# Performance work log

Measured on AMD Instinct MI355X. Metric: run time of the kernel, lower is better.

Reference implementation:

```python
import jax, jax.numpy as jnp
import numpy as np

N, E, D_IN, D, L = 50000, 800000, 128, 256, 3
BN_EPS = 1e-5


def _bn(x, gamma, beta):
    # torch BatchNorm1d training-mode forward: biased batch statistics over node dim
    m = x.mean(axis=0)
    v = x.var(axis=0)  # ddof=0, matches torch normalization
    return gamma * (x - m) * jax.lax.rsqrt(v + BN_EPS) + beta


def setup_inputs() -> dict:
    key = jax.random.key(0)
    ks = jax.random.split(key, 12)
    s_in = 1.0 / np.sqrt(D_IN)
    s_d = 1.0 / np.sqrt(D)
    s_2d = 1.0 / np.sqrt(2 * D)
    return {
        "pre_node_emb": jax.random.normal(ks[0], (1, N, D_IN), jnp.float32),
        "edge_index": jax.random.randint(ks[1], (1, E, 2), 0, N, jnp.int64),
        "W0": jax.random.uniform(ks[2], (D_IN, D), jnp.float32, -s_in, s_in),
        "b0": jax.random.uniform(ks[3], (D,), jnp.float32, -s_in, s_in),
        "W1": jax.random.uniform(ks[4], (L, D, 2 * D), jnp.float32, -s_d, s_d),
        "b1": jax.random.uniform(ks[5], (L, 2 * D), jnp.float32, -s_d, s_d),
        "g1": jnp.ones((L, 2 * D), jnp.float32),
        "beta1": jnp.zeros((L, 2 * D), jnp.float32),
        "W2": jax.random.uniform(ks[6], (L, 2 * D, D), jnp.float32, -s_2d, s_2d),
        "b2": jax.random.uniform(ks[7], (L, D), jnp.float32, -s_2d, s_2d),
        "gf": jnp.ones((L, D), jnp.float32),
        "betaf": jnp.zeros((L, D), jnp.float32),
    }


def reference(pre_node_emb, edge_index, W0, b0, W1, b1, g1, beta1, W2, b2, gf, betaf):
    x = pre_node_emb[0]            # [N, D_IN]
    ei = edge_index[0]             # [E, 2] -> transposed in torch; rows are (src, dst)
    src, dst = ei[:, 0], ei[:, 1]
    x = x @ W0 + b0                # node embedder -> [N, D]
    for l in range(L):
        # GINConv (eps=0): sum-aggregate neighbor messages, then MLP
        agg = jax.ops.segment_sum(x[src], dst, num_segments=N)   # scatter-add
        h = x + agg
        h = h @ W1[l] + b1[l]
        h = _bn(h, g1[l], beta1[l])
        h = jax.nn.relu(h)
        h = h @ W2[l] + b2[l]
        x = _bn(h + x, gf[l], betaf[l])  # residual + outer BatchNorm
    return x
```

## Files before the change

### kernel.cpp

```cpp
#include <hip/hip_runtime.h>

#define MNODES 50000
#define M_PAD  50048
#define NEDGES 800000
#define DIN    128
#define DD     256
#define D2     512
#define NLAYERS 3
#define BN_EPS 1e-5f
#define NREP   16

typedef unsigned short ushort_t;
typedef __bf16 v8bf __attribute__((ext_vector_type(8)));
typedef unsigned short v8us __attribute__((ext_vector_type(8)));
typedef float  v4f  __attribute__((ext_vector_type(4)));

#define GLOBAL_AS __attribute__((address_space(1)))
#define LDS_AS    __attribute__((address_space(3)))

__device__ __forceinline__ float bf2f(ushort_t u) {
    unsigned x = ((unsigned)u) << 16;
    return __uint_as_float(x);
}
__device__ __forceinline__ ushort_t f2bf(float f) {
    unsigned u = __float_as_uint(f);
    u += 0x7FFF + ((u >> 16) & 1);
    return (ushort_t)(u >> 16);
}
__device__ __forceinline__ void async16(const ushort_t* g, ushort_t* l) {
    __builtin_amdgcn_global_load_lds((const GLOBAL_AS unsigned int*)g,
                                     (LDS_AS unsigned int*)l, 16, 0, 0);
}
#define BARRIER() asm volatile("s_barrier" ::: "memory")
#define VMWAIT4() asm volatile("s_waitcnt vmcnt(4)" ::: "memory")
#define VMWAIT0() asm volatile("s_waitcnt vmcnt(0)" ::: "memory")
#define LGKM0()   asm volatile("s_waitcnt lgkmcnt(0)" ::: "memory")

#define R0 (M_PAD * DIN)
#define RW (DIN * DD + 2 * NLAYERS * DD * D2)
#define NSTATZ (NREP * D2 * 2 + NREP * DD * 2)
__global__ void k_prep_all(const float* __restrict__ pre, ushort_t* __restrict__ preb,
                           const float* __restrict__ W0, const float* __restrict__ W1,
                           const float* __restrict__ W2,
                           ushort_t* __restrict__ W0T, ushort_t* __restrict__ W1T,
                           ushort_t* __restrict__ W2T,
                           float* __restrict__ caf, float* __restrict__ ccf,
                           float* __restrict__ statz, int* __restrict__ deg) {
    int i = blockIdx.x * blockDim.x + threadIdx.x;
    if (i < R0) {
        int row = i >> 7;
        preb[i] = f2bf(row < MNODES ? pre[i] : 0.f);
        return;
    }
    int j = i - R0;
    if (j < RW) {
        if (j < DIN * DD) {
            int n = j >> 7, k = j & 127;
            W0T[j] = f2bf(W0[k * DD + n]);
        } else if (j < DIN * DD + NLAYERS * DD * D2) {
            int j2 = j - DIN * DD;
            int l = j2 >> 17, off = j2 & 131071;
            int n = off >> 8, k = off & 255;
            W1T[(size_t)l * 131072 + off] = f2bf(W1[(size_t)l * 131072 + k * D2 + n]);
        } else {
            int j2 = j - DIN * DD - NLAYERS * DD * D2;
            int l = j2 >> 17, off = j2 & 131071;
            int n = off >> 9, k = off & 511;
            W2T[(size_t)l * 131072 + off] = f2bf(W2[(size_t)l * 131072 + k * DD + n]);
        }
        return;
    }
    j -= RW;
    if (j < 256) { caf[j] = 1.f; ccf[j] = 0.f; return; }
    j -= 256;
    if (j < NSTATZ) { statz[j] = 0.f; return; }
    j -= NSTATZ;
    if (j < MNODES) deg[j] = 0;
}

__global__ void k_hist(const int* __restrict__ ei, int* __restrict__ deg) {
    int e = blockIdx.x * blockDim.x + threadIdx.x;
    if (e < NEDGES) atomicAdd(&deg[ei[e * 2 + 1]], 1);
}
__global__ void k_scan1(const int* __restrict__ deg, int* __restrict__ rowptr,
                        int* __restrict__ bsum, int n) {
    __shared__ int tmp[256];
    int tid = threadIdx.x;
    int i = blockIdx.x * 256 + tid;
    int v = (i < n) ? deg[i] : 0;
    tmp[tid] = v;
    __syncthreads();
    #pragma unroll
    for (int off = 1; off < 256; off <<= 1) {
        int t = (tid >= off) ? tmp[tid - off] : 0;
        __syncthreads();
        tmp[tid] += t;
        __syncthreads();
    }
    if (i < n) rowptr[i + 1] = tmp[tid];
    if (tid == 255) bsum[blockIdx.x] = tmp[255];
}
__global__ __launch_bounds__(256)
void k_scan2(int* __restrict__ bsum, int nb) {
    __shared__ int tmp[256];
    int tid = threadIdx.x;
    int v = (tid < nb) ? bsum[tid] : 0;
    tmp[tid] = v;
    __syncthreads();
    #pragma unroll
    for (int off = 1; off < 256; off <<= 1) {
        int t = (tid >= off) ? tmp[tid - off] : 0;
        __syncthreads();
        tmp[tid] += t;
        __syncthreads();
    }
    if (tid < nb) bsum[tid] = tmp[tid] - v;
}
__global__ void k_scan3(const int* __restrict__ deg, const int* __restrict__ bsum,
                        int* __restrict__ rowptr, int* __restrict__ cursor, int n) {
    int i = blockIdx.x * 256 + threadIdx.x;
    if (i == 0) rowptr[0] = 0;
    if (i < n) {
        int incl = rowptr[i + 1] + bsum[i >> 8];
        rowptr[i + 1] = incl;
        cursor[i] = incl - deg[i];
    }
}
__global__ void k_fill(const int* __restrict__ ei, int* __restrict__ cursor,
                       int* __restrict__ col) {
    int e = blockIdx.x * blockDim.x + threadIdx.x;
    if (e < NEDGES) {
        int pos = atomicAdd(&cursor[ei[e * 2 + 1]], 1);
        col[pos] = ei[e * 2];
    }
}

__global__ void k_gather(const int* __restrict__ rowptr, const int* __restrict__ col,
                         const ushort_t* __restrict__ x, const float* __restrict__ ca,
                         const float* __restrict__ cc, ushort_t* __restrict__ out) {
    int node = blockIdx.x * 4 + (threadIdx.x >> 6);
    int lane = threadIdx.x & 63;
    if (node >= MNODES) return;
    const ushort4* xp = (const ushort4*)x;
    ushort4 v = xp[(size_t)node * 64 + lane];
    float a0 = bf2f(v.x), a1 = bf2f(v.y), a2 = bf2f(v.z), a3 = bf2f(v.w);
    int s = rowptr[node], e = rowptr[node + 1];
    int i = s;
    for (; i + 7 < e; i += 8) {
        ushort4 u[8];
        #pragma unroll
        for (int j = 0; j < 8; j++) u[j] = xp[(size_t)col[i + j] * 64 + lane];
        #pragma unroll
        for (int j = 0; j < 8; j++) {
            a0 += bf2f(u[j].x); a1 += bf2f(u[j].y);
            a2 += bf2f(u[j].z); a3 += bf2f(u[j].w);
        }
    }
    for (; i < e; i++) {
        ushort4 u = xp[(size_t)col[i] * 64 + lane];
        a0 += bf2f(u.x); a1 += bf2f(u.y); a2 += bf2f(u.z); a3 += bf2f(u.w);
    }
    int c = lane * 4;
    float dn = (float)(e - s) + 1.0f;
    ushort4 o;
    o.x = f2bf(ca[c + 0] * a0 + dn * cc[c + 0]);
    o.y = f2bf(ca[c + 1] * a1 + dn * cc[c + 1]);
    o.z = f2bf(ca[c + 2] * a2 + dn * cc[c + 2]);
    o.w = f2bf(ca[c + 3] * a3 + dn * cc[c + 3]);
    ((ushort4*)out)[(size_t)node * 64 + lane] = o;
}

__global__ void k_coeffs(float* __restrict__ sums, float* __restrict__ sumsq,
                         const float* __restrict__ g, const float* __restrict__ beta,
                         float* __restrict__ ca, float* __restrict__ cc,
                         float2* __restrict__ cacc, int n) {
    int c = blockIdx.x * blockDim.x + threadIdx.x;
    if (c >= n) return;
    float s = 0.f, q = 0.f;
    #pragma unroll
    for (int r = 0; r < NREP; r++) {
        s += sums[r * n + c];  sums[r * n + c]  = 0.f;
        q += sumsq[r * n + c]; sumsq[r * n + c] = 0.f;
    }
    float mean = s * (1.0f / MNODES);
    float var  = q * (1.0f / MNODES) - mean * mean;
    float a    = g[c] * rsqrtf(var + BN_EPS);
    float b    = beta[c] - a * mean;
    ca[c] = a;
    cc[c] = b;
    if (cacc) cacc[c] = make_float2(a, b);
}

__global__ void k_apply_out(const ushort_t* __restrict__ h, const float* __restrict__ ca,
                            const float* __restrict__ cc, float* __restrict__ out) {
    int i = blockIdx.x * blockDim.x + threadIdx.x;
    if (i >= MNODES * 64) return;
    int c = (i & 63) * 4;
    ushort4 v = ((const ushort4*)h)[i];
    float4 o;
    o.x = ca[c + 0] * bf2f(v.x) + cc[c + 0];
    o.y = ca[c + 1] * bf2f(v.y) + cc[c + 1];
    o.z = ca[c + 2] * bf2f(v.z) + cc[c + 2];
    o.w = ca[c + 3] * bf2f(v.w) + cc[c + 3];
    ((float4*)out)[i] = o;
}

template<int DO_STATS, int RES, int FUSE_BN>
__global__ __launch_bounds__(256, 4)
void k_gemm_bf(const ushort_t* __restrict__ A, const ushort_t* __restrict__ WT,
               const float* __restrict__ bias,
               const ushort_t* resid, const float* __restrict__ r_ca,
               const float* __restrict__ r_cc, const float2* __restrict__ cacc,
               ushort_t* out, float* __restrict__ sums, float* __restrict__ sumsq,
               int M, int K, int N) {
    __shared__ __align__(16) ushort_t As[2][128 * 32];
    __shared__ __align__(16) ushort_t Bs[2][128 * 32];
    const int tid = threadIdx.x;
    const int w = tid >> 6, lane = tid & 63;
    const int wm = w >> 1, wn = w & 1;
    const int quad = lane >> 4, l15 = lane & 15;

    const int nxb = N >> 7;
    const int nwg = nxb * (int)gridDim.y;
    const int orig = (int)blockIdx.y * nxb + (int)blockIdx.x;
    const int qq = nwg >> 3, rr = nwg & 7, xc = orig & 7, oi = orig >> 3;
    const int swz = (xc < rr ? xc * (qq + 1) : rr * (qq + 1) + (xc - rr) * qq) + oi;
    const int bx = swz & (nxb - 1);
    const int by = (nxb == 4) ? (swz >> 2) : (swz >> 1);
    const int m0 = by * 128, n0 = bx * 128;

    float2* cacc_lds = nullptr;
    if constexpr (FUSE_BN != 0) {
        __shared__ __align__(16) float2 cacc_s[512];
        cacc_lds = cacc_s;
        for (int k2 = tid; k2 < K; k2 += 256) cacc_lds[k2] = cacc[k2];
        LGKM0();
    }

    const ushort_t* aA[2];
    const ushort_t* aB[2];
    int aoff[2];
    #pragma unroll
    for (int j = 0; j < 2; j++) {
        int ii = j * 4 + w;
        int r = ii * 16 + (lane >> 2);
        int cg = (lane & 3) ^ ((r >> 2) & 3);
        aA[j] = A  + (size_t)(m0 + r) * K + cg * 8;
        aB[j] = WT + (size_t)(n0 + r) * K + cg * 8;
        aoff[j] = ii * 512;
    }

    v4f acc[4][4];
    #pragma unroll
    for (int i = 0; i < 4; i++)
        #pragma unroll
        for (int j = 0; j < 4; j++)
            acc[i][j] = (v4f){0.f, 0.f, 0.f, 0.f};

    const int nk = K >> 5;

    #pragma unroll
    for (int j = 0; j < 2; j++) {
        async16(aA[j], &As[0][aoff[j]]);
        async16(aB[j], &Bs[0][aoff[j]]);
    }
    #pragma unroll
    for (int j = 0; j < 2; j++) {
        async16(aA[j] + 32, &As[1][aoff[j]]);
        async16(aB[j] + 32, &Bs[1][aoff[j]]);
    }
    VMWAIT4();
    BARRIER();

    const int sl = quad ^ ((l15 >> 2) & 3);
    for (int t = 0; t < nk; t++) {
        const ushort_t* Ab = As[t & 1];
        const ushort_t* Bb = Bs[t & 1];
        v8bf af[4], bfr[4];
        #pragma unroll
        for (int tt = 0; tt < 4; tt++) {
            int m_l = wm * 64 + tt * 16 + l15;
            af[tt]  = *(const v8bf*)&Ab[m_l * 32 + sl * 8];
            int n_l = wn * 64 + tt * 16 + l15;
            bfr[tt] = *(const v8bf*)&Bb[n_l * 32 + sl * 8];
        }
        if constexpr (FUSE_BN != 0) {
            const float* cb = (const float*)&cacc_lds[(t << 5) + (quad << 3)];
            float cav[8], ccv[8];
            #pragma unroll
            for (int j = 0; j < 8; j++) { cav[j] = cb[2 * j]; ccv[j] = cb[2 * j + 1]; }
            #pragma unroll
            for (int tt = 0; tt < 4; tt++) {
                v8us au = *(v8us*)&af[tt];
                v8us ou;
                #pragma unroll
                for (int j = 0; j < 8; j++) {
                    float h = bf2f(au[j]);
                    ou[j] = f2bf(fmaxf(fmaf(cav[j], h, ccv[j]), 0.f));
                }
                af[tt] = *(v8bf*)&ou;
            }
        }
        #pragma unroll
        for (int mt = 0; mt < 4; mt++)
            #pragma unroll
            for (int nt = 0; nt < 4; nt++)
                acc[mt][nt] = __builtin_amdgcn_mfma_f32_16x16x32_bf16(
                    af[mt], bfr[nt], acc[mt][nt], 0, 0, 0);
        if (t == nk - 1) break;
        BARRIER();
        if (t + 2 < nk) {
            int kl = (t + 2) * 32;
            #pragma unroll
            for (int j = 0; j < 2; j++) {
                async16(aA[j] + kl, &As[t & 1][aoff[j]]);
                async16(aB[j] + kl, &Bs[t & 1][aoff[j]]);
            }
            VMWAIT4();
        } else {
            VMWAIT0();
        }
        BARRIER();
    }

    const int mlim = M - m0;
    float s_sum[4] = {0.f, 0.f, 0.f, 0.f}, s_sq[4] = {0.f, 0.f, 0.f, 0.f};
    #pragma unroll
    for (int nt = 0; nt < 4; nt++) {
        int colg = n0 + wn * 64 + nt * 16 + l15;
        float bia = bias[colg];
        float rca = 0.f, rcc = 0.f;
        if (RES) { rca = r_ca[colg]; rcc = r_cc[colg]; }
        #pragma unroll
        for (int mt = 0; mt < 4; mt++) {
            int rbase = wm * 64 + mt * 16 + quad * 4;
            #pragma unroll
            for (int r = 0; r < 4; r++) {
                int rl = rbase + r;
                if (rl < mlim) {
                    size_t idx = (size_t)(m0 + rl) * N + colg;
                    float v = acc[mt][nt][r] + bia;
                    if (RES) v += rca * bf2f(resid[idx]) + rcc;
                    out[idx] = f2bf(v);
                    if (DO_STATS) { s_sum[nt] += v; s_sq[nt] += v * v; }
                }
            }
        }
    }
    if (DO_STATS) {
        const int rep = by & (NREP - 1);
        #pragma unroll
        for (int nt = 0; nt < 4; nt++) {
            float s = s_sum[nt], q = s_sq[nt];
            s += __shfl_xor(s, 16); q += __shfl_xor(q, 16);
            s += __shfl_xor(s, 32); q += __shfl_xor(q, 32);
            if (quad == 0) {
                int colg = n0 + wn * 64 + nt * 16 + l15;
                atomicAdd(&sums[rep * N + colg], s);
                atomicAdd(&sumsq[rep * N + colg], q);
            }
        }
    }
}

extern "C" void kernel_launch(void* const* d_in, const int* in_sizes, int n_in,
                              void* d_out, int out_size, void* d_ws, size_t ws_size,
                              hipStream_t stream) {
    const float* pre   = (const float*)d_in[0];
    const int*   ei    = (const int*)d_in[1];
    const float* W0    = (const float*)d_in[2];
    const float* b0    = (const float*)d_in[3];
    const float* W1    = (const float*)d_in[4];
    const float* b1    = (const float*)d_in[5];
    const float* g1    = (const float*)d_in[6];
    const float* beta1 = (const float*)d_in[7];
    const float* W2    = (const float*)d_in[8];
    const float* b2    = (const float*)d_in[9];
    const float* gf    = (const float*)d_in[10];
    const float* betaf = (const float*)d_in[11];

    char* p = (char*)d_ws;
    ushort_t* preb = (ushort_t*)p; p += (size_t)M_PAD * DIN * 2;
    ushort_t* ACT1 = (ushort_t*)p; p += (size_t)M_PAD * DD * 2;
    ushort_t* ACT2 = (ushort_t*)p; p += (size_t)M_PAD * DD * 2;
    ushort_t* H1   = (ushort_t*)p; p += (size_t)M_PAD * D2 * 2;
    ushort_t* W0T  = (ushort_t*)p; p += (size_t)DIN * DD * 2;
    ushort_t* W1T  = (ushort_t*)p; p += (size_t)NLAYERS * DD * D2 * 2;
    ushort_t* W2T  = (ushort_t*)p; p += (size_t)NLAYERS * D2 * DD * 2;
    float* sums1  = (float*)p; p += (size_t)NREP * D2 * 4;
    float* sumsq1 = (float*)p; p += (size_t)NREP * D2 * 4;
    float* sumsF  = (float*)p; p += (size_t)NREP * DD * 4;
    float* sumsqF = (float*)p; p += (size_t)NREP * DD * 4;
    float* ca1    = (float*)p; p += D2 * 4;
    float* cc1    = (float*)p; p += D2 * 4;
    float* caf    = (float*)p; p += DD * 4;
    float* ccf    = (float*)p; p += DD * 4;
    float2* cacc1 = (float2*)p; p += D2 * 8;
    int* deg    = (int*)p; p += (size_t)MNODES * 4;
    int* rowptr = (int*)p; p += (size_t)(MNODES + 1) * 4;
    int* cursor = (int*)p; p += (size_t)MNODES * 4;
    int* colx   = (int*)p; p += (size_t)NEDGES * 4;
    int* bsum   = (int*)p; p += 256 * 4;

    dim3 blk(256);
    const int mb = (MNODES + 127) / 128;
    const int nsb = (MNODES + 255) / 256;

    const int prep_total = R0 + RW + 256 + NSTATZ + MNODES;
    k_prep_all<<<(prep_total + 255) / 256, blk, 0, stream>>>(
        pre, preb, W0, W1, W2, W0T, W1T, W2T, caf, ccf, sums1, deg);

    k_hist<<<(NEDGES + 255) / 256, blk, 0, stream>>>(ei, deg);
    k_scan1<<<nsb, blk, 0, stream>>>(deg, rowptr, bsum, MNODES);
    k_scan2<<<1, blk, 0, stream>>>(bsum, nsb);
    k_scan3<<<nsb, blk, 0, stream>>>(deg, bsum, rowptr, cursor, MNODES);
    k_fill<<<(NEDGES + 255) / 256, blk, 0, stream>>>(ei, cursor, colx);

    k_gemm_bf<0, 0, 0><<<dim3(DD / 128, mb), blk, 0, stream>>>(
        preb, W0T, b0, nullptr, nullptr, nullptr, nullptr,
        ACT2, nullptr, nullptr, MNODES, DIN, DD);

    for (int l = 0; l < NLAYERS; l++) {
        k_gather<<<(MNODES + 3) / 4, blk, 0, stream>>>(rowptr, colx, ACT2, caf, ccf, ACT1);

        k_gemm_bf<1, 0, 0><<<dim3(D2 / 128, mb), blk, 0, stream>>>(
            ACT1, W1T + (size_t)l * DD * D2, b1 + (size_t)l * D2,
            nullptr, nullptr, nullptr, nullptr,
            H1, sums1, sumsq1, MNODES, DD, D2);
        k_coeffs<<<2, blk, 0, stream>>>(sums1, sumsq1, g1 + (size_t)l * D2,
                                        beta1 + (size_t)l * D2, ca1, cc1, cacc1, D2);

        k_gemm_bf<1, 1, 1><<<dim3(DD / 128, mb), blk, 0, stream>>>(
            H1, W2T + (size_t)l * D2 * DD, b2 + (size_t)l * DD,
            ACT2, caf, ccf, cacc1,
            ACT2, sumsF, sumsqF, MNODES, D2, DD);
        k_coeffs<<<1, blk, 0, stream>>>(sumsF, sumsqF, gf + (size_t)l * DD,
                                        betaf + (size_t)l * DD, caf, ccf, nullptr, DD);
    }

    k_apply_out<<<(MNODES * 64 + 255) / 256, blk, 0, stream>>>(ACT2, caf, ccf, (float*)d_out);
}
```

Before: 749.4 us.

## Load GEMM fragments directly from global memory into registers, bypassing LDS

The bf16 MFMA GEMM no longer stages A and B tiles in double-buffered LDS with async global-to-LDS copies and barriers. Each wave now loads its own A and B fragments straight from global memory into registers, with a two-stage register ping-pong for A. K becomes a template parameter so loop bounds and strides are compile-time constants. This removes LDS traffic and barrier synchronisation, but rows shared between waves are loaded redundantly through the caches, B fragments are fetched just before use with little latency hiding, and accesses are less coalesced.

Measured after the change: 1.264 ms. 68.7% more time.

```diff
diff --git a/kernel.cpp b/kernel.cpp
--- a/kernel.cpp
+++ b/kernel.cpp
@@ -15,9 +15,6 @@
 typedef unsigned short v8us __attribute__((ext_vector_type(8)));
 typedef float  v4f  __attribute__((ext_vector_type(4)));
 
-#define GLOBAL_AS __attribute__((address_space(1)))
-#define LDS_AS    __attribute__((address_space(3)))
-
 __device__ __forceinline__ float bf2f(ushort_t u) {
     unsigned x = ((unsigned)u) << 16;
     return __uint_as_float(x);
@@ -27,13 +24,6 @@
     u += 0x7FFF + ((u >> 16) & 1);
     return (ushort_t)(u >> 16);
 }
-__device__ __forceinline__ void async16(const ushort_t* g, ushort_t* l) {
-    __builtin_amdgcn_global_load_lds((const GLOBAL_AS unsigned int*)g,
-                                     (LDS_AS unsigned int*)l, 16, 0, 0);
-}
-#define BARRIER() asm volatile("s_barrier" ::: "memory")
-#define VMWAIT4() asm volatile("s_waitcnt vmcnt(4)" ::: "memory")
-#define VMWAIT0() asm volatile("s_waitcnt vmcnt(0)" ::: "memory")
 #define LGKM0()   asm volatile("s_waitcnt lgkmcnt(0)" ::: "memory")
 
 #define R0 (M_PAD * DIN)
@@ -205,16 +195,14 @@
     ((float4*)out)[i] = o;
 }
 
-template<int DO_STATS, int RES, int FUSE_BN>
+template<int DO_STATS, int RES, int FUSE_BN, int KT>
 __global__ __launch_bounds__(256, 4)
 void k_gemm_bf(const ushort_t* __restrict__ A, const ushort_t* __restrict__ WT,
                const float* __restrict__ bias,
                const ushort_t* resid, const float* __restrict__ r_ca,
                const float* __restrict__ r_cc, const float2* __restrict__ cacc,
                ushort_t* out, float* __restrict__ sums, float* __restrict__ sumsq,
-               int M, int K, int N) {
-    __shared__ __align__(16) ushort_t As[2][128 * 32];
-    __shared__ __align__(16) ushort_t Bs[2][128 * 32];
+               int M, int N) {
     const int tid = threadIdx.x;
     const int w = tid >> 6, lane = tid & 63;
     const int wm = w >> 1, wn = w & 1;
@@ -231,24 +219,15 @@
 
     float2* cacc_lds = nullptr;
     if constexpr (FUSE_BN != 0) {
-        __shared__ __align__(16) float2 cacc_s[512];
+        __shared__ __align__(16) float2 cacc_s[KT];
         cacc_lds = cacc_s;
-        for (int k2 = tid; k2 < K; k2 += 256) cacc_lds[k2] = cacc[k2];
-        LGKM0();
-    }
-
-    const ushort_t* aA[2];
-    const ushort_t* aB[2];
-    int aoff[2];
-    #pragma unroll
-    for (int j = 0; j < 2; j++) {
-        int ii = j * 4 + w;
-        int r = ii * 16 + (lane >> 2);
-        int cg = (lane & 3) ^ ((r >> 2) & 3);
-        aA[j] = A  + (size_t)(m0 + r) * K + cg * 8;
-        aB[j] = WT + (size_t)(n0 + r) * K + cg * 8;
-        aoff[j] = ii * 512;
-    }
+        #pragma unroll
+        for (int k2 = tid; k2 < KT; k2 += 256) cacc_lds[k2] = cacc[k2];
+        __syncthreads();
+    }
+
+    const ushort_t* Ap = A  + (size_t)(m0 + wm * 64 + l15) * KT + quad * 8;
+    const ushort_t* Bp = WT + (size_t)(n0 + wn * 64 + l15) * KT + quad * 8;
 
     v4f acc[4][4];
     #pragma unroll
@@ -257,48 +236,31 @@
         for (int j = 0; j < 4; j++)
             acc[i][j] = (v4f){0.f, 0.f, 0.f, 0.f};
 
-    const int nk = K >> 5;
-
-    #pragma unroll
-    for (int j = 0; j < 2; j++) {
-        async16(aA[j], &As[0][aoff[j]]);
-        async16(aB[j], &Bs[0][aoff[j]]);
-    }
-    #pragma unroll
-    for (int j = 0; j < 2; j++) {
-        async16(aA[j] + 32, &As[1][aoff[j]]);
-        async16(aB[j] + 32, &Bs[1][aoff[j]]);
-    }
-    VMWAIT4();
-    BARRIER();
-
-    const int sl = quad ^ ((l15 >> 2) & 3);
-    for (int t = 0; t < nk; t++) {
-        const ushort_t* Ab = As[t & 1];
-        const ushort_t* Bb = Bs[t & 1];
-        v8bf af[4], bfr[4];
-        #pragma unroll
-        for (int tt = 0; tt < 4; tt++) {
-            int m_l = wm * 64 + tt * 16 + l15;
-            af[tt]  = *(const v8bf*)&Ab[m_l * 32 + sl * 8];
-            int n_l = wn * 64 + tt * 16 + l15;
-            bfr[tt] = *(const v8bf*)&Bb[n_l * 32 + sl * 8];
-        }
+    constexpr int nk = KT >> 5;
+
+    v8bf aP[4], aQ[4];
+    #pragma unroll
+    for (int tt = 0; tt < 4; tt++) aP[tt] = *(const v8bf*)(Ap + tt * 16 * KT);
+    #pragma unroll
+    for (int tt = 0; tt < 4; tt++) aQ[tt] = *(const v8bf*)(Ap + tt * 16 * KT + 32);
+
+    for (int t = 0; t < nk; t += 2) {
+        v8bf bb[4];
+        #pragma unroll
+        for (int tt = 0; tt < 4; tt++)
+            bb[tt] = *(const v8bf*)(Bp + tt * 16 * KT + t * 32);
         if constexpr (FUSE_BN != 0) {
             const float* cb = (const float*)&cacc_lds[(t << 5) + (quad << 3)];
-            float cav[8], ccv[8];
-            #pragma unroll
-            for (int j = 0; j < 8; j++) { cav[j] = cb[2 * j]; ccv[j] = cb[2 * j + 1]; }
             #pragma unroll
             for (int tt = 0; tt < 4; tt++) {
-                v8us au = *(v8us*)&af[tt];
-                v8us ou;
+                v8us au = *(v8us*)&aP[tt];
+                v8bf o;
                 #pragma unroll
                 for (int j = 0; j < 8; j++) {
                     float h = bf2f(au[j]);
-                    ou[j] = f2bf(fmaxf(fmaf(cav[j], h, ccv[j]), 0.f));
+                    o[j] = (__bf16)fmaxf(fmaf(cb[2 * j], h, cb[2 * j + 1]), 0.f);
                 }
-                af[tt] = *(v8bf*)&ou;
+                aP[tt] = o;
             }
         }
         #pragma unroll
@@ -306,21 +268,40 @@
             #pragma unroll
             for (int nt = 0; nt < 4; nt++)
                 acc[mt][nt] = __builtin_amdgcn_mfma_f32_16x16x32_bf16(
-                    af[mt], bfr[nt], acc[mt][nt], 0, 0, 0);
-        if (t == nk - 1) break;
-        BARRIER();
+                    aP[mt], bb[nt], acc[mt][nt], 0, 0, 0);
         if (t + 2 < nk) {
-            int kl = (t + 2) * 32;
-            #pragma unroll
-            for (int j = 0; j < 2; j++) {
-                async16(aA[j] + kl, &As[t & 1][aoff[j]]);
-                async16(aB[j] + kl, &Bs[t & 1][aoff[j]]);
+            #pragma unroll
+            for (int tt = 0; tt < 4; tt++)
+                aP[tt] = *(const v8bf*)(Ap + tt * 16 * KT + (t + 2) * 32);
+        }
+        #pragma unroll
+        for (int tt = 0; tt < 4; tt++)
+            bb[tt] = *(const v8bf*)(Bp + tt * 16 * KT + (t + 1) * 32);
+        if constexpr (FUSE_BN != 0) {
+            const float* cb = (const float*)&cacc_lds[((t + 1) << 5) + (quad << 3)];
+            #pragma unroll
+            for (int tt = 0; tt < 4; tt++) {
+                v8us au = *(v8us*)&aQ[tt];
+                v8bf o;
+                #pragma unroll
+                for (int j = 0; j < 8; j++) {
+                    float h = bf2f(au[j]);
+                    o[j] = (__bf16)fmaxf(fmaf(cb[2 * j], h, cb[2 * j + 1]), 0.f);
+                }
+                aQ[tt] = o;
             }
-            VMWAIT4();
-        } else {
-            VMWAIT0();
-        }
-        BARRIER();
+        }
+        #pragma unroll
+        for (int mt = 0; mt < 4; mt++)
+            #pragma unroll
+            for (int nt = 0; nt < 4; nt++)
+                acc[mt][nt] = __builtin_amdgcn_mfma_f32_16x16x32_bf16(
+                    aQ[mt], bb[nt], acc[mt][nt], 0, 0, 0);
+        if (t + 3 < nk) {
+            #pragma unroll
+            for (int tt = 0; tt < 4; tt++)
+                aQ[tt] = *(const v8bf*)(Ap + tt * 16 * KT + (t + 3) * 32);
+        }
     }
 
     const int mlim = M - m0;
@@ -416,24 +397,24 @@
     k_scan3<<<nsb, blk, 0, stream>>>(deg, bsum, rowptr, cursor, MNODES);
     k_fill<<<(NEDGES + 255) / 256, blk, 0, stream>>>(ei, cursor, colx);
 
-    k_gemm_bf<0, 0, 0><<<dim3(DD / 128, mb), blk, 0, stream>>>(
+    k_gemm_bf<0, 0, 0, DIN><<<dim3(DD / 128, mb), blk, 0, stream>>>(
         preb, W0T, b0, nullptr, nullptr, nullptr, nullptr,
-        ACT2, nullptr, nullptr, MNODES, DIN, DD);
+        ACT2, nullptr, nullptr, MNODES, DD);
 
     for (int l = 0; l < NLAYERS; l++) {
         k_gather<<<(MNODES + 3) / 4, blk, 0, stream>>>(rowptr, colx, ACT2, caf, ccf, ACT1);
 
-        k_gemm_bf<1, 0, 0><<<dim3(D2 / 128, mb), blk, 0, stream>>>(
+        k_gemm_bf<1, 0, 0, DD><<<dim3(D2 / 128, mb), blk, 0, stream>>>(
             ACT1, W1T + (size_t)l * DD * D2, b1 + (size_t)l * D2,
             nullptr, nullptr, nullptr, nullptr,
-            H1, sums1, sumsq1, MNODES, DD, D2);
+            H1, sums1, sumsq1, MNODES, D2);
         k_coeffs<<<2, blk, 0, stream>>>(sums1, sumsq1, g1 + (size_t)l * D2,
                                         beta1 + (size_t)l * D2, ca1, cc1, cacc1, D2);
 
-        k_gemm_bf<1, 1, 1><<<dim3(DD / 128, mb), blk, 0, stream>>>(
+        k_gemm_bf<1, 1, 1, D2><<<dim3(DD / 128, mb), blk, 0, stream>>>(
             H1, W2T + (size_t)l * D2 * DD, b2 + (size_t)l * DD,
             ACT2, caf, ccf, cacc1,
-            ACT2, sumsF, sumsqF, MNODES, D2, DD);
+            ACT2, sumsF, sumsqF, MNODES, DD);
         k_coeffs<<<1, blk, 0, stream>>>(sumsF, sumsqF, gf + (size_t)l * DD,
                                         betaf + (size_t)l * DD, caf, ccf, nullptr, DD);
     }
```
